# Optimization experiments

Measured on AMD Instinct MI355X. Metric: run time of the kernel, lower is better.

The kernel has to match this reference:

```python
import jax, jax.numpy as jnp
import numpy as np

B = 8; C = 256; NH = 8; CH = C // NH; MLP_H = 4 * C; EPS = 1e-5
SIZES = [(56, 56), (28, 28), (14, 14), (7, 7)]  # scales 2..5; scale1 (112x112) passes through


def _layernorm(x, g, b):
    mu = jnp.mean(x, -1, keepdims=True)
    var = jnp.mean((x - mu) ** 2, -1, keepdims=True)
    return (x - mu) * jax.lax.rsqrt(var + EPS) * g + b


def _dwconv(x, w, b, pad):
    # x: [B, C, H, W], w: [C, 1, k, k] depthwise
    out = jax.lax.conv_general_dilated(
        x, w, (1, 1), [(pad, pad), (pad, pad)],
        feature_group_count=x.shape[1],
        dimension_numbers=('NCHW', 'OIHW', 'NCHW'))
    return out + b[None, :, None, None]


def _cpe(x, w, b, size):
    # ConvPosEnc: depthwise 3x3 conv residual on image tokens, cls untouched
    Hh, Ww = size
    Bb, N, Cc = x.shape
    cls_tok, img = x[:, :1], x[:, 1:]
    feat = img.transpose(0, 2, 1).reshape(Bb, Cc, Hh, Ww)
    feat = _dwconv(feat, w, b, 1) + feat
    img = feat.reshape(Bb, Cc, Hh * Ww).transpose(0, 2, 1)
    return jnp.concatenate([cls_tok, img], axis=1)


def _crpe(q, v, ws, bs, size):
    # ConvRelPosEnc: window->head split {3:2, 5:3, 7:3}; EV_hat = q * dwconv(v)
    Hh, Ww = size
    Bb, h, N, Ch = q.shape
    q_img, v_img = q[:, :, 1:], v[:, :, 1:]
    v_map = v_img.transpose(0, 1, 3, 2).reshape(Bb, h * Ch, Hh, Ww)
    splits = [2 * Ch, 3 * Ch, 3 * Ch]
    start = 0; outs = []
    for i, win in enumerate((3, 5, 7)):
        part = v_map[:, start:start + splits[i]]
        outs.append(_dwconv(part, ws[i], bs[i], win // 2))
        start += splits[i]
    conv_v = jnp.concatenate(outs, 1).reshape(Bb, h, Ch, Hh * Ww).transpose(0, 1, 3, 2)
    ev = q_img * conv_v  # [B, h, HW, Ch]
    return jnp.pad(ev, ((0, 0), (0, 0), (1, 0), (0, 0)))  # zero row for cls token


def _factor_att(x, qkv_w, proj_w, proj_b, crpe_ws, crpe_bs, size):
    Bb, N, Cc = x.shape
    qkv = (x @ qkv_w.T).reshape(Bb, N, 3, NH, CH).transpose(2, 0, 3, 1, 4)
    q, k, v = qkv[0], qkv[1], qkv[2]
    k_sm = jax.nn.softmax(k, axis=2)                       # softmax over tokens
    kv = jnp.einsum('bhnk,bhnv->bhkv', k_sm, v)            # [B,h,Ch,Ch]
    fa = jnp.einsum('bhnk,bhkv->bhnv', q, kv)              # [B,h,N,Ch]
    cr = _crpe(q, v, crpe_ws, crpe_bs, size)
    out = (CH ** -0.5 * fa + cr).transpose(0, 2, 1, 3).reshape(Bb, N, Cc)
    return out @ proj_w.T + proj_b


def _interp(x, out_size, size):
    # bilinear (align_corners=False) on image tokens; cls token passes through
    Bb, N, Cc = x.shape
    Hh, Ww = size
    cls_tok, img = x[:, :1], x[:, 1:]
    feat = img.transpose(0, 2, 1).reshape(Bb, Cc, Hh, Ww)
    feat = jax.image.resize(feat, (Bb, Cc, out_size[0], out_size[1]),
                            method='bilinear', antialias=False)
    img = feat.reshape(Bb, Cc, -1).transpose(0, 2, 1)
    return jnp.concatenate([cls_tok, img], axis=1)


def _mlp(x, w1, b1, w2, b2):
    h = jax.nn.gelu(x @ w1.T + b1, approximate=False)
    return h @ w2.T + b2


def _forward(x1, x2, x3, x4, x5, cpe_w, cpe_b, n1_g, n1_b, qkv_w, proj_w, proj_b,
             crpe_w3, crpe_b3, crpe_w5, crpe_b5, crpe_w7, crpe_b7,
             n2_g, n2_b, fc1_w, fc1_b, fc2_w, fc2_b):
    xs = [x2, x3, x4, x5]
    curs = []
    for i in range(4):  # fixed set of 4 scales (not a data-dim loop)
        xi = _cpe(xs[i], cpe_w[i], cpe_b[i], SIZES[i])
        cur = _layernorm(xi, n1_g[i], n1_b[i])
        cur = _factor_att(cur, qkv_w[i], proj_w[i], proj_b[i],
                          (crpe_w3[i], crpe_w5[i], crpe_w7[i]),
                          (crpe_b3[i], crpe_b5[i], crpe_b7[i]), SIZES[i])
        xs[i] = xi
        curs.append(cur)
    c2, c3, c4, c5 = curs
    s2, s3, s4, s5 = SIZES
    # only the interpolations actually used in the residual sums (source has dead ones)
    c2n = c2 + _interp(c3, s2, s3) + _interp(c4, s2, s4)
    c3n = c3 + _interp(c4, s3, s4) + _interp(c2, s3, s2)
    c4n = c4 + _interp(c5, s4, s5) + _interp(c2, s4, s2)
    c5n = c5 + _interp(c4, s5, s4) + _interp(c2, s5, s2)
    curs = [c2n, c3n, c4n, c5n]
    for i in range(4):
        xs[i] = xs[i] + curs[i]
        cur = _layernorm(xs[i], n2_g[i], n2_b[i])
        cur = _mlp(cur, fc1_w, fc1_b, fc2_w, fc2_b)  # MLP shared across scales
        xs[i] = xs[i] + cur
    return (x1, xs[0], xs[1], xs[2], xs[3])


def setup_inputs() -> dict:
    key = jax.random.key(0)
    ks = iter(jax.random.split(key, 40))
    def nrm(shape, scale=1.0):
        return jax.random.normal(next(ks), shape, jnp.float32) * scale
    W = 0.02
    inp = {}
    inp['x1'] = nrm((B, 1 + 112 * 112, C))
    for j, (h, w) in enumerate(SIZES):
        inp['x%d' % (j + 2)] = nrm((B, 1 + h * w, C))
    inp['cpe_w'] = nrm((4, C, 1, 3, 3), W); inp['cpe_b'] = jnp.zeros((4, C))
    inp['n1_g'] = jnp.ones((4, C)); inp['n1_b'] = jnp.zeros((4, C))
    inp['qkv_w'] = nrm((4, 3 * C, C), W)
    inp['proj_w'] = nrm((4, C, C), W); inp['proj_b'] = jnp.zeros((4, C))
    inp['crpe_w3'] = nrm((4, 2 * CH, 1, 3, 3), W); inp['crpe_b3'] = jnp.zeros((4, 2 * CH))
    inp['crpe_w5'] = nrm((4, 3 * CH, 1, 5, 5), W); inp['crpe_b5'] = jnp.zeros((4, 3 * CH))
    inp['crpe_w7'] = nrm((4, 3 * CH, 1, 7, 7), W); inp['crpe_b7'] = jnp.zeros((4, 3 * CH))
    inp['n2_g'] = jnp.ones((4, C)); inp['n2_b'] = jnp.zeros((4, C))
    inp['fc1_w'] = nrm((MLP_H, C), W); inp['fc1_b'] = jnp.zeros((MLP_H,))
    inp['fc2_w'] = nrm((C, MLP_H), W); inp['fc2_b'] = jnp.zeros((C,))
    return inp


def reference(x1, x2, x3, x4, x5, cpe_w, cpe_b, n1_g, n1_b, qkv_w, proj_w, proj_b,
              crpe_w3, crpe_b3, crpe_w5, crpe_b5, crpe_w7, crpe_b7,
              n2_g, n2_b, fc1_w, fc1_b, fc2_w, fc2_b):
    return _forward(x1, x2, x3, x4, x5, cpe_w, cpe_b, n1_g, n1_b, qkv_w, proj_w, proj_b,
                    crpe_w3, crpe_b3, crpe_w5, crpe_b5, crpe_w7, crpe_b7,
                    n2_g, n2_b, fc1_w, fc1_b, fc2_w, fc2_b)
```

## Files before the change

### kernel.cpp

```cpp
#include <hip/hip_runtime.h>
#include <math.h>

typedef unsigned short u16;
typedef __attribute__((ext_vector_type(8))) short bf16x8;
typedef __attribute__((ext_vector_type(4))) float f32x4;

#define MP 36864
#define OUTOFF0 25692160ull

#define DEV __device__ __forceinline__
#define AS1 __attribute__((address_space(1)))
#define AS3 __attribute__((address_space(3)))

DEV u16 f2bf(float x) {
  union { float f; unsigned u; } v; v.f = x;
  unsigned r = v.u + 0x7fffu + ((v.u >> 16) & 1u);
  return (u16)(r >> 16);
}
DEV float bf2f(u16 x) {
  union { unsigned u; float f; } v; v.u = ((unsigned)x) << 16;
  return v.f;
}

struct alignas(8) u16x4s { u16 x, y, z, w; };
struct alignas(16) U16x8 { u16 d[8]; };

DEV int rs_s(int row)   { return (row >= 25600) + (row >= 33792) + (row >= 35840); }
DEV int selPB(int s)    { return s == 0 ? 0 : s == 1 ? 25600 : s == 2 ? 33792 : 35840; }
DEV int selNPAD(int s)  { return s == 0 ? 3200 : s == 1 ? 1024 : s == 2 ? 256 : 128; }
DEV int selN(int s)     { return s == 0 ? 3137 : s == 1 ? 785 : s == 2 ? 197 : 50; }
DEV int selH(int s)     { return s == 0 ? 56 : s == 1 ? 28 : s == 2 ? 14 : 7; }
DEV int selRO(int s)    { return s == 0 ? 0 : s == 1 ? 25096 : s == 2 ? 31376 : 32952; }
DEV size_t selKPB(int s){ return s == 0 ? 0ull : s == 1 ? 6553600ull : s == 2 ? 8650752ull : 9175040ull; }
DEV size_t selVPB(int s){ return s == 0 ? 0ull : s == 1 ? 7340032ull : s == 2 ? 11010048ull : 12845056ull; }
DEV int selNC(int s)    { return s == 0 ? 32 : s == 1 ? 8 : s == 2 ? 2 : 1; }
DEV int selNCB(int s)   { return s == 0 ? 0 : s == 1 ? 2048 : s == 2 ? 2560 : 2688; }
DEV unsigned selHM(int s){ return s == 0 ? 74899u : s == 1 ? 149797u : s == 2 ? 299594u : 599187u; }

DEV void sbn(int row, int s, int& b, int& n) {
  int l = row - selPB(s);
  if (s == 0)      { b = l / 3200; n = l - b * 3200; }
  else if (s == 1) { b = l >> 10; n = l & 1023; }
  else if (s == 2) { b = l >> 8;  n = l & 255; }
  else             { b = l >> 7;  n = l & 127; }
}

DEV int xcd_swizzle(int orig, int nblk) {
  int q = nblk >> 3, r = nblk & 7;
  int xcd = orig & 7, lin = orig >> 3;
  return (xcd < r ? xcd * (q + 1) : r * (q + 1) + (xcd - r) * q) + lin;
}

__global__ void cvt_bf16(const float* __restrict__ src, u16* __restrict__ dst, int n) {
  for (int i = blockIdx.x * blockDim.x + threadIdx.x; i < n; i += gridDim.x * blockDim.x)
    dst[i] = f2bf(src[i]);
}

__global__ void tpw_cpe(const float* __restrict__ src, float* __restrict__ dst) {
  int i = blockIdx.y;
  int e = blockIdx.x * 256 + threadIdx.x;
  if (e < 2304) {
    int c = e / 9, k = e % 9;
    dst[i * 2304 + k * 256 + c] = src[i * 2304 + c * 9 + k];
  }
}

__global__ void copy_f4(const float4* __restrict__ src, float4* __restrict__ dst, int n4) {
  for (int i = blockIdx.x * blockDim.x + threadIdx.x; i < n4; i += gridDim.x * blockDim.x)
    dst[i] = src[i];
}

__global__ void cpe_ln_all(const float* __restrict__ x2, const float* __restrict__ x3,
                           const float* __restrict__ x4, const float* __restrict__ x5,
                           const float* __restrict__ WT, const float* __restrict__ cpe_b,
                           const float* __restrict__ n1g, const float* __restrict__ n1b,
                           float* __restrict__ XI, u16* __restrict__ T1) {
  int wid = threadIdx.x >> 6, lane = threadIdx.x & 63;
  int row = blockIdx.x * 4 + wid;
  if (row >= MP) return;
  int s = rs_s(row);
  int b, n; sbn(row, s, b, n);
  int N = selN(s), H = selH(s);
  int c4 = lane * 4;
  float4 v = make_float4(0.f, 0.f, 0.f, 0.f);
  if (n < N) {
    const float* x = s == 0 ? x2 : s == 1 ? x3 : s == 2 ? x4 : x5;
    v = *(const float4*)(x + ((size_t)b * N + n) * 256 + c4);
    if (n > 0) {
      int p = n - 1, h0 = p / H, w0 = p % H;
      float4 acc = *(const float4*)(cpe_b + s * 256 + c4);
      const float* wT = WT + s * 2304;
      #pragma unroll
      for (int kh = 0; kh < 3; ++kh) {
        int hh = h0 + kh - 1;
        if (hh < 0 || hh >= H) continue;
        #pragma unroll
        for (int kw = 0; kw < 3; ++kw) {
          int ww = w0 + kw - 1;
          if (ww < 0 || ww >= H) continue;
          float4 t = *(const float4*)(x + ((size_t)b * N + 1 + hh * H + ww) * 256 + c4);
          float4 wv = *(const float4*)(wT + (kh * 3 + kw) * 256 + c4);
          acc.x += t.x * wv.x; acc.y += t.y * wv.y;
          acc.z += t.z * wv.z; acc.w += t.w * wv.w;
        }
      }
      v.x += acc.x; v.y += acc.y; v.z += acc.z; v.w += acc.w;
    }
  }
  *(float4*)(XI + (size_t)row * 256 + c4) = v;
  float sm = v.x + v.y + v.z + v.w;
  #pragma unroll
  for (int off = 32; off; off >>= 1) sm += __shfl_down(sm, off);
  sm = __shfl(sm, 0);
  float mu = sm * (1.0f / 256.0f);
  float dx = v.x - mu, dy = v.y - mu, dz = v.z - mu, dw = v.w - mu;
  float q = dx * dx + dy * dy + dz * dz + dw * dw;
  #pragma unroll
  for (int off = 32; off; off >>= 1) q += __shfl_down(q, off);
  q = __shfl(q, 0);
  float rs = rsqrtf(q * (1.0f / 256.0f) + 1e-5f);
  float4 gg = *(const float4*)(n1g + s * 256 + c4);
  float4 bb = *(const float4*)(n1b + s * 256 + c4);
  u16x4s o;
  o.x = f2bf(dx * rs * gg.x + bb.x);
  o.y = f2bf(dy * rs * gg.y + bb.y);
  o.z = f2bf(dz * rs * gg.z + bb.z);
  o.w = f2bf(dw * rs * gg.w + bb.w);
  *(u16x4s*)(T1 + (size_t)row * 256 + c4) = o;
}

DEV void stage32(const u16* __restrict__ A, const u16* __restrict__ W,
                 u16* dst, int bm, int bn, int K, int k0) {
  int t = threadIdx.x, wv = t >> 6;
  u16* aD = dst;
  u16* bD = dst + 4096;
  #pragma unroll
  for (int iss = 0; iss < 2; ++iss) {
    int sI = iss * 256 + t;
    int row = sI >> 2, g = sI & 3;
    int gel = ((g ^ (row & 3)) << 3);
    __builtin_amdgcn_global_load_lds(
        (const AS1 void*)(A + (size_t)(bm + row) * K + k0 + gel),
        (AS3 void*)(aD + (size_t)(iss * 256 + wv * 64) * 8), 16, 0, 0);
    __builtin_amdgcn_global_load_lds(
        (const AS1 void*)(W + (size_t)(bn + row) * K + k0 + gel),
        (AS3 void*)(bD + (size_t)(iss * 256 + wv * 64) * 8), 16, 0, 0);
  }
}

DEV void mainloop(const u16* __restrict__ A, const u16* __restrict__ W, int K,
                  int bm, int bn, u16* lds, f32x4 (&acc)[4][4]) {
  int t = threadIdx.x, lane = t & 63, wv = t >> 6;
  int wr = wv >> 1, wc = wv & 1;
  const int nt = K >> 5;
  stage32(A, W, lds, bm, bn, K, 0);
  for (int tt = 0; tt < nt; ++tt) {
    __syncthreads();
    if (tt + 1 < nt) stage32(A, W, lds + ((tt + 1) & 1) * 8192, bm, bn, K, (tt + 1) << 5);
    const u16* aS = lds + (tt & 1) * 8192;
    const u16* bS = aS + 4096;
    bf16x8 af[4], bfr[4];
    #pragma unroll
    for (int m = 0; m < 4; ++m) {
      int row = wr * 64 + m * 16 + (lane & 15);
      int sg = (lane >> 4) ^ (row & 3);
      af[m] = *(const bf16x8*)(aS + row * 32 + sg * 8);
    }
    #pragma unroll
    for (int n = 0; n < 4; ++n) {
      int row = wc * 64 + n * 16 + (lane & 15);
      int sg = (lane >> 4) ^ (row & 3);
      bfr[n] = *(const bf16x8*)(bS + row * 32 + sg * 8);
    }
    #pragma unroll
    for (int m = 0; m < 4; ++m)
      #pragma unroll
      for (int n = 0; n < 4; ++n)
        acc[m][n] = __builtin_amdgcn_mfma_f32_16x16x32_bf16(af[m], bfr[n], acc[m][n], 0, 0, 0);
  }
}

DEV void epi_dump(const f32x4 (&acc)[4][4], int pass, float* eps) {
  int t = threadIdx.x, lane = t & 63, wv = t >> 6;
  int wr = wv >> 1, wc = wv & 1;
  if (wr != (pass >> 1)) return;
  #pragma unroll
  for (int mh = 0; mh < 2; ++mh) {
    int m = (pass & 1) * 2 + mh;
    #pragma unroll
    for (int n = 0; n < 4; ++n) {
      int col = wc * 64 + n * 16 + (lane & 15);
      #pragma unroll
      for (int rg = 0; rg < 4; ++rg)
        eps[(mh * 16 + ((lane >> 4) << 2) + rg) * 132 + col] = acc[m][n][rg];
    }
  }
}

template <bool GELU, bool BF16>
DEV void epi_rowmajor(const float* eps, int pass, void* outp, const float* bias,
                      int bm, int bn, int Nout) {
  int t = threadIdx.x;
  int lr = t >> 3, cb = (t & 7) * 4;
  int gr = bm + pass * 32 + lr;
  #pragma unroll
  for (int j = 0; j < 4; ++j) {
    int col = cb + j * 32;
    float4 f = *(const float4*)(eps + lr * 132 + col);
    int gc = bn + col;
    if (bias) {
      float4 bv = *(const float4*)(bias + gc);
      f.x += bv.x; f.y += bv.y; f.z += bv.z; f.w += bv.w;
    }
    if (GELU) {
      f.x /= (1.0f + __expf(-1.702f * f.x));
      f.y /= (1.0f + __expf(-1.702f * f.y));
      f.z /= (1.0f + __expf(-1.702f * f.z));
      f.w /= (1.0f + __expf(-1.702f * f.w));
    }
    if (BF16) {
      u16x4s p;
      p.x = f2bf(f.x); p.y = f2bf(f.y); p.z = f2bf(f.z); p.w = f2bf(f.w);
      *(u16x4s*)((u16*)outp + (size_t)gr * Nout + gc) = p;
    } else {
      *(float4*)((float*)outp + (size_t)gr * Nout + gc) = f;
    }
  }
}

template <bool GELU, bool BF16>
__launch_bounds__(256, 4)
__global__ void gemm_std(const u16* __restrict__ A, const u16* __restrict__ W,
                         const float* __restrict__ bias, void* __restrict__ outp,
                         int K, int Nout, int nnt) {
  __shared__ __align__(16) u16 lds[16384];
  int wg = xcd_swizzle(blockIdx.x, gridDim.x);
  int bm = (wg / nnt) << 7, bn = (wg % nnt) << 7;
  f32x4 acc[4][4] = {};
  mainloop(A, W, K, bm, bn, lds, acc);
  float* eps = (float*)lds;
  #pragma unroll
  for (int pass = 0; pass < 4; ++pass) {
    __syncthreads();
    epi_dump(acc, pass, eps);
    __syncthreads();
    epi_rowmajor<GELU, BF16>(eps, pass, outp, bias, bm, bn, Nout);
  }
}

__launch_bounds__(256, 4)
__global__ void qkv_gemm(const u16* __restrict__ A, const u16* __restrict__ WQ,
                         u16* __restrict__ Q16, u16* __restrict__ KP,
                         u16* __restrict__ VP, u16* __restrict__ VPI) {
  __shared__ __align__(16) u16 lds[16384];
  int wg = xcd_swizzle(blockIdx.x, gridDim.x);
  int mt = wg / 6, ct = wg % 6;
  int bm = mt << 7, bn = ct << 7;
  int s = rs_s(bm);
  f32x4 acc[4][4] = {};
  mainloop(A, WQ + (size_t)s * 196608, 256, bm, bn, lds, acc);
  float* eps = (float*)lds;
  int b, nb; sbn(bm, s, b, nb);
  int NPAD = selNPAD(s), H = selH(s), HW = H * H;
  unsigned hmag = selHM(s);
  #pragma unroll
  for (int pass = 0; pass < 4; ++pass) {
    __syncthreads();
    epi_dump(acc, pass, eps);
    __syncthreads();
    if (ct < 2) {
      epi_rowmajor<false, true>(eps, pass, Q16, nullptr, bm, bn, 256);
    } else {
      int t = threadIdx.x;
      int c = t >> 1, half = t & 1;
      bool isK = (ct < 4);
      int cg = bn - (isK ? 256 : 512) + c;
      int n0 = nb + pass * 32 + half * 16;
      float vals[16];
      #pragma unroll
      for (int r = 0; r < 16; ++r) vals[r] = eps[(half * 16 + r) * 132 + c];
      U16x8 p0, p1;
      #pragma unroll
      for (int e = 0; e < 8; ++e) { p0.d[e] = f2bf(vals[e]); p1.d[e] = f2bf(vals[8 + e]); }
      u16* pbase = (isK ? KP : VP) + selKPB(s) + (size_t)(b * 256 + cg) * NPAD + n0;
      *(U16x8*)pbase = p0;
      *(U16x8*)(pbase + 8) = p1;
      if (!isK) {
        u16* vplane = VPI + selVPB(s) + (size_t)(b * 256 + cg) * (H * 64);
        #pragma unroll
        for (int r = 0; r < 16; ++r) {
          int n = n0 + r;
          if (n >= 1 && n <= HW) {
            int p = n - 1;
            int qd = (int)(((unsigned)p * hmag) >> 22);
            vplane[qd * 64 + (p - qd * H)] = f2bf(vals[r]);
          }
        }
      }
    }
  }
}

__launch_bounds__(256, 4)
__global__ void proj_gemm(const u16* __restrict__ A, const u16* __restrict__ WP,
                          const float* __restrict__ proj_b, float* __restrict__ CC) {
  __shared__ __align__(16) u16 lds[16384];
  int wg = xcd_swizzle(blockIdx.x, gridDim.x);
  int bm = (wg >> 1) << 7, bn = (wg & 1) << 7;
  int s = rs_s(bm);
  f32x4 acc[4][4] = {};
  mainloop(A, WP + (size_t)s * 65536, 256, bm, bn, lds, acc);
  float* eps = (float*)lds;
  #pragma unroll
  for (int pass = 0; pass < 4; ++pass) {
    __syncthreads();
    epi_dump(acc, pass, eps);
    __syncthreads();
    epi_rowmajor<false, false>(eps, pass, CC, proj_b + s * 256, bm, bn, 256);
  }
}

__launch_bounds__(256, 4)
__global__ void fc2_gemm(const u16* __restrict__ A, const u16* __restrict__ W2,
                         const float* __restrict__ fc2_b, const float* __restrict__ XI,
                         float* __restrict__ out) {
  __shared__ __align__(16) u16 lds[16384];
  int wg = xcd_swizzle(blockIdx.x, gridDim.x);
  int bm = (wg >> 1) << 7, bn = (wg & 1) << 7;
  f32x4 acc[4][4] = {};
  mainloop(A, W2, 1024, bm, bn, lds, acc);
  float* eps = (float*)lds;
  int s = rs_s(bm);
  int b, nb; sbn(bm, s, b, nb);
  int N = selN(s), RO = selRO(s);
  #pragma unroll
  for (int pass = 0; pass < 4; ++pass) {
    __syncthreads();
    epi_dump(acc, pass, eps);
    __syncthreads();
    int t = threadIdx.x;
    int lr = t >> 3, cb = (t & 7) * 4;
    int n = nb + pass * 32 + lr;
    if (n >= N) continue;
    int prow = bm + pass * 32 + lr;
    size_t orow = (size_t)RO + (size_t)b * N + n;
    #pragma unroll
    for (int j = 0; j < 4; ++j) {
      int col = cb + j * 32;
      float4 f = *(const float4*)(eps + lr * 132 + col);
      int gc = bn + col;
      float4 bv = *(const float4*)(fc2_b + gc);
      float4 rv = *(const float4*)(XI + (size_t)prow * 256 + gc);
      f.x += bv.x + rv.x; f.y += bv.y + rv.y;
      f.z += bv.z + rv.z; f.w += bv.w + rv.w;
      *(float4*)(out + OUTOFF0 + orow * 256 + gc) = f;
    }
  }
}

__global__ void ksm_all(const u16* __restrict__ KP, float* __restrict__ mx,
                        float* __restrict__ se) {
  int s = blockIdx.z, b = blockIdx.y;
  int N = selN(s), NPAD = selNPAD(s);
  int wv = threadIdx.x >> 6, lane = threadIdx.x & 63;
  int cg = blockIdx.x * 4 + wv;
  const u16* kp = KP + selKPB(s) + (size_t)(b * 256 + cg) * NPAD;
  float m = -1e30f, sm = 0.f;
  for (int n = lane; n < N; n += 64) {
    float v = bf2f(kp[n]);
    float nm = fmaxf(m, v);
    sm = sm * __expf(m - nm) + __expf(v - nm);
    m = nm;
  }
  #pragma unroll
  for (int off = 1; off < 64; off <<= 1) {
    float mo = __shfl_xor(m, off), so = __shfl_xor(sm, off);
    float nm = fmaxf(m, mo);
    sm = sm * __expf(m - nm) + so * __expf(mo - nm);
    m = nm;
  }
  if (lane == 0) { mx[s * 2048 + b * 256 + cg] = m; se[s * 2048 + b * 256 + cg] = sm; }
}

__launch_bounds__(1024)
__global__ void kv_partial_all(const u16* __restrict__ KP, const u16* __restrict__ VP,
                               const float* __restrict__ mx, float* __restrict__ part) {
  __shared__ float kl[32][65];
  __shared__ float vl[32][65];
  int blk = blockIdx.x;
  int s = (blk >= selNCB(1)) + (blk >= selNCB(2)) + (blk >= selNCB(3));
  int local = blk - selNCB(s);
  int NC = selNC(s);
  int chunk = local % NC;
  int bh = local / NC;
  int b = bh >> 3, h = bh & 7;
  int N = selN(s), NPAD = selNPAD(s);
  int chunkrows = (N + NC - 1) / NC;
  const u16* kpb = KP + selKPB(s);
  const u16* vpb = VP + selKPB(s);
  int t = threadIdx.x;
  int i = t >> 5, j = t & 31;
  float acc = 0.f;
  int n0s = chunk * chunkrows, n1s = min(N, n0s + chunkrows);
  for (int n0 = n0s; n0 < n1s; n0 += 64) {
    #pragma unroll
    for (int e = t; e < 2048; e += 1024) {
      int c = e >> 6, nn = e & 63;
      int n = n0 + nn;
      bool ok = (n < n1s);
      kl[c][nn] = ok ? bf2f(kpb[(size_t)(b * 256 + h * 32 + c) * NPAD + n]) : -1e30f;
      vl[c][nn] = ok ? bf2f(vpb[(size_t)(b * 256 + h * 32 + c) * NPAD + n]) : 0.f;
    }
    __syncthreads();
    #pragma unroll
    for (int e = t; e < 2048; e += 1024) {
      int c = e >> 6, nn = e & 63;
      kl[c][nn] = __expf(kl[c][nn] - mx[s * 2048 + b * 256 + h * 32 + c]);
    }
    __syncthreads();
    #pragma unroll
    for (int nn = 0; nn < 64; ++nn) acc += kl[i][nn] * vl[j][nn];
    __syncthreads();
  }
  part[(size_t)blk * 1024 + t] = acc;
}

__global__ void kv_reduce_all(const float* __restrict__ part, const float* __restrict__ se,
                              float* __restrict__ kv) {
  int bh = blockIdx.x, s = blockIdx.y;
  int NC = selNC(s), base = selNCB(s);
  int t = threadIdx.x;
  int i = t >> 5;
  int b = bh >> 3, h = bh & 7;
  float sm = 0.f;
  for (int c = 0; c < NC; ++c) sm += part[(size_t)(base + bh * NC + c) * 1024 + t];
  kv[(size_t)s * 65536 + bh * 1024 + t] = sm / se[s * 2048 + b * 256 + h * 32 + i];
}

template <int KS, int C0>
__global__ void crpe_all(const u16* __restrict__ VPI, const float* __restrict__ w,
                         const float* __restrict__ bias, u16* __restrict__ CVPI, int CS) {
  constexpr int pad = KS / 2;
  int z = blockIdx.z;
  int s = (z >= 2) + (z >= 3) + (z >= 4);
  int sub = z - (s == 0 ? 0 : s + 1);
  int RS = (s == 0) ? 2 : 1;
  int H = selH(s);
  int c = blockIdx.x, b = blockIdx.y;
  int G = (H + 7) >> 3;
  int hpb = (H + RS - 1) / RS;
  int h0b = sub * hpb;
  int h1b = min(H, h0b + hpb);
  size_t plane = selVPB(s) + (size_t)(b * 256 + C0 + c) * (size_t)(H * 64);
  const u16* vp = VPI + plane;
  u16* op = CVPI + plane;
  float wreg[KS * KS];
  #pragma unroll
  for (int e = 0; e < KS * KS; ++e) wreg[e] = w[(s * CS + c) * KS * KS + e];
  float bb = bias[s * CS + c];
  int ntask = (h1b - h0b) * G;
  for (int task = threadIdx.x; task < ntask; task += 256) {
    int g = task % G;
    int h = h0b + task / G;
    int w0 = g << 3;
    float o[8];
    #pragma unroll
    for (int e = 0; e < 8; ++e) o[e] = bb;
    #pragma unroll
    for (int kh = 0; kh < KS; ++kh) {
      int hh = h + kh - pad;
      if (hh < 0 || hh >= H) continue;
      const u16* rowp = vp + hh * 64;
      U16x8 ch0 = {}, ch1, ch2;
      if (w0 >= 8) ch0 = *(const U16x8*)(rowp + w0 - 8);
      ch1 = *(const U16x8*)(rowp + w0);
      ch2 = *(const U16x8*)(rowp + w0 + 8);
      float tv[24];
      #pragma unroll
      for (int j2 = 8 - pad; j2 <= 15 + pad; ++j2) {
        u16 raw = (j2 < 8) ? ch0.d[j2] : (j2 < 16 ? ch1.d[j2 - 8] : ch2.d[j2 - 16]);
        tv[j2] = bf2f(raw);
      }
      #pragma unroll
      for (int kw = 0; kw < KS; ++kw) {
        float wv = wreg[kh * KS + kw];
        #pragma unroll
        for (int e = 0; e < 8; ++e) o[e] += tv[8 + e + kw - pad] * wv;
      }
    }
    U16x8 pk;
    #pragma unroll
    for (int e = 0; e < 8; ++e) pk.d[e] = f2bf(o[e]);
    *(U16x8*)(op + h * 64 + w0) = pk;
  }
}

__global__ void att_all(const u16* __restrict__ Q16, const u16* __restrict__ CVPI,
                        const float* __restrict__ kvg, u16* __restrict__ attp) {
  int s = blockIdx.z, b = blockIdx.y;
  int N = selN(s), H = selH(s);
  int n0 = blockIdx.x * 16;
  if (n0 >= N) return;
  __shared__ float kvl[8192];
  __shared__ float ql[256];
  __shared__ float cl[16][260];
  int t = threadIdx.x;
  int hw64 = H * 64;
  size_t rowbase = (size_t)selPB(s) + (size_t)b * selNPAD(s);
  const u16* cvb = CVPI + selVPB(s);
  for (int e = t; e < 8192; e += 256) kvl[e] = kvg[(size_t)s * 65536 + b * 8192 + e];
  for (int e = t; e < 4096; e += 256) {
    int c = e >> 4, nn = e & 15;
    int n = n0 + nn;
    float v = 0.f;
    if (n >= 1 && n < N) {
      int p = n - 1;
      v = bf2f(cvb[(size_t)(b * 256 + c) * hw64 + (p / H) * 64 + (p % H)]);
    }
    cl[nn][c] = v;
  }
  int h = t >> 5, j = t & 31;
  for (int nn = 0; nn < 16; ++nn) {
    int n = n0 + nn;
    if (n >= N) break;
    __syncthreads();
    ql[t] = bf2f(Q16[(rowbase + n) * 256 + t]);
    __syncthreads();
    float fa = 0.f;
    const float* kvh = kvl + h * 1024;
    #pragma unroll
    for (int k = 0; k < 32; ++k) fa += ql[h * 32 + k] * kvh[k * 32 + j];
    float v = 0.17677669529663687f * fa + ql[t] * cl[nn][t];
    attp[(rowbase + n) * 256 + t] = f2bf(v);
  }
}

DEV float4 bs4(const float* __restrict__ base, int Hs, int oh, int ow, int Hi, int c4) {
  float scale = (float)Hs / (float)Hi;
  float sy = (oh + 0.5f) * scale - 0.5f;
  float sx = (ow + 0.5f) * scale - 0.5f;
  float fy0 = floorf(sy), fx0 = floorf(sx);
  float fy = sy - fy0, fx = sx - fx0;
  int y0 = (int)fy0, x0 = (int)fx0;
  int y0c = min(max(y0, 0), Hs - 1), y1c = min(max(y0 + 1, 0), Hs - 1);
  int x0c = min(max(x0, 0), Hs - 1), x1c = min(max(x0 + 1, 0), Hs - 1);
  const float* ib = base + 256 + c4;
  float4 v00 = *(const float4*)(ib + (size_t)(y0c * Hs + x0c) * 256);
  float4 v01 = *(const float4*)(ib + (size_t)(y0c * Hs + x1c) * 256);
  float4 v10 = *(const float4*)(ib + (size_t)(y1c * Hs + x0c) * 256);
  float4 v11 = *(const float4*)(ib + (size_t)(y1c * Hs + x1c) * 256);
  float w00 = (1.f - fy) * (1.f - fx), w01 = (1.f - fy) * fx;
  float w10 = fy * (1.f - fx), w11 = fy * fx;
  float4 r;
  r.x = w00 * v00.x + w01 * v01.x + w10 * v10.x + w11 * v11.x;
  r.y = w00 * v00.y + w01 * v01.y + w10 * v10.y + w11 * v11.y;
  r.z = w00 * v00.z + w01 * v01.z + w10 * v10.z + w11 * v11.z;
  r.w = w00 * v00.w + w01 * v01.w + w10 * v10.w + w11 * v11.w;
  return r;
}

__global__ void combine_ln_all(float* __restrict__ XI, const float* __restrict__ CC,
                               const float* __restrict__ n2g, const float* __restrict__ n2b,
                               u16* __restrict__ T1) {
  int wid = threadIdx.x >> 6, lane = threadIdx.x & 63;
  int row = blockIdx.x * 4 + wid;
  if (row >= MP) return;
  int s = rs_s(row);
  int b, n; sbn(row, s, b, n);
  int N = selN(s), Hi = selH(s);
  int c4 = lane * 4;
  float4 v;
  if (n < N) {
    float4 add = *(const float4*)(CC + (size_t)row * 256 + c4);
    int sa = s == 0 ? 1 : s == 1 ? 2 : s == 2 ? 3 : 2;
    int sb_ = s == 0 ? 2 : 0;
    const float* baseA = CC + ((size_t)selPB(sa) + (size_t)b * selNPAD(sa)) * 256;
    const float* baseB = CC + ((size_t)selPB(sb_) + (size_t)b * selNPAD(sb_)) * 256;
    if (n == 0) {
      float4 a = *(const float4*)(baseA + c4);
      float4 bb2 = *(const float4*)(baseB + c4);
      add.x += a.x + bb2.x; add.y += a.y + bb2.y;
      add.z += a.z + bb2.z; add.w += a.w + bb2.w;
    } else {
      int p = n - 1, oh = p / Hi, ow = p % Hi;
      float4 a = bs4(baseA, selH(sa), oh, ow, Hi, c4);
      float4 bb2 = bs4(baseB, selH(sb_), oh, ow, Hi, c4);
      add.x += a.x + bb2.x; add.y += a.y + bb2.y;
      add.z += a.z + bb2.z; add.w += a.w + bb2.w;
    }
    float* xp = XI + (size_t)row * 256 + c4;
    v = *(const float4*)xp;
    v.x += add.x; v.y += add.y; v.z += add.z; v.w += add.w;
    *(float4*)xp = v;
  } else {
    v = make_float4(0.f, 0.f, 0.f, 0.f);
  }
  float sm = v.x + v.y + v.z + v.w;
  #pragma unroll
  for (int off = 32; off; off >>= 1) sm += __shfl_down(sm, off);
  sm = __shfl(sm, 0);
  float mu = sm * (1.0f / 256.0f);
  float dx = v.x - mu, dy = v.y - mu, dz = v.z - mu, dw = v.w - mu;
  float q = dx * dx + dy * dy + dz * dz + dw * dw;
  #pragma unroll
  for (int off = 32; off; off >>= 1) q += __shfl_down(q, off);
  q = __shfl(q, 0);
  float rs = rsqrtf(q * (1.0f / 256.0f) + 1e-5f);
  float4 gg = *(const float4*)(n2g + s * 256 + c4);
  float4 bb = *(const float4*)(n2b + s * 256 + c4);
  u16x4s o;
  o.x = f2bf(dx * rs * gg.x + bb.x);
  o.y = f2bf(dy * rs * gg.y + bb.y);
  o.z = f2bf(dz * rs * gg.z + bb.z);
  o.w = f2bf(dw * rs * gg.w + bb.w);
  *(u16x4s*)(T1 + (size_t)row * 256 + c4) = o;
}

extern "C" void kernel_launch(void* const* d_in, const int* in_sizes, int n_in,
                              void* d_out, int out_size, void* d_ws, size_t ws_size,
                              hipStream_t stream) {
  const float* x1 = (const float*)d_in[0];
  const float* x2 = (const float*)d_in[1];
  const float* x3 = (const float*)d_in[2];
  const float* x4 = (const float*)d_in[3];
  const float* x5 = (const float*)d_in[4];
  const float* cpe_w  = (const float*)d_in[5];
  const float* cpe_b  = (const float*)d_in[6];
  const float* n1_g   = (const float*)d_in[7];
  const float* n1_b   = (const float*)d_in[8];
  const float* qkv_w  = (const float*)d_in[9];
  const float* proj_w = (const float*)d_in[10];
  const float* proj_b = (const float*)d_in[11];
  const float* crpe_w3 = (const float*)d_in[12];
  const float* crpe_b3 = (const float*)d_in[13];
  const float* crpe_w5 = (const float*)d_in[14];
  const float* crpe_b5 = (const float*)d_in[15];
  const float* crpe_w7 = (const float*)d_in[16];
  const float* crpe_b7 = (const float*)d_in[17];
  const float* n2_g   = (const float*)d_in[18];
  const float* n2_b   = (const float*)d_in[19];
  const float* fc1_w  = (const float*)d_in[20];
  const float* fc1_b  = (const float*)d_in[21];
  const float* fc2_w  = (const float*)d_in[22];
  const float* fc2_b  = (const float*)d_in[23];

  float* ws = (float*)d_ws;
  float* XI   = ws;
  float* CC   = XI + 9437184;
  u16*   T1   = (u16*)(CC + 9437184);
  float* REG  = (float*)(T1 + 9437184);
  u16*   Q16  = (u16*)REG;
  u16*   KP   = Q16 + 9437184;
  u16*   VP   = KP + 9437184;
  u16*   VPI  = VP + 9437184;
  u16*   CVPI = VPI + 13762560;
  float* PRT  = (float*)CVPI;
  u16*   T2   = (u16*)REG;
  float* MX   = (float*)(CVPI + 13762560);
  float* SE   = MX + 8192;
  float* KV   = SE + 8192;
  u16*   WQ   = (u16*)(KV + 262144);
  u16*   WP   = WQ + 786432;
  u16*   W1   = WP + 262144;
  u16*   W2   = W1 + 262144;
  float* WT   = (float*)(W2 + 262144);

  float* out = (float*)d_out;

  hipMemsetAsync(VPI, 0, 13762560ull * 2, stream);
  cvt_bf16<<<1536, 256, 0, stream>>>(qkv_w, WQ, 786432);
  cvt_bf16<<<512, 256, 0, stream>>>(proj_w, WP, 262144);
  cvt_bf16<<<512, 256, 0, stream>>>(fc1_w, W1, 262144);
  cvt_bf16<<<512, 256, 0, stream>>>(fc2_w, W2, 262144);
  tpw_cpe<<<dim3(9, 4), 256, 0, stream>>>(cpe_w, WT);

  copy_f4<<<8192, 256, 0, stream>>>((const float4*)x1, (float4*)out, 25692160 / 4);

  cpe_ln_all<<<MP / 4, 256, 0, stream>>>(x2, x3, x4, x5, WT, cpe_b, n1_g, n1_b, XI, T1);

  qkv_gemm<<<288 * 6, 256, 0, stream>>>(T1, WQ, Q16, KP, VP, VPI);

  ksm_all<<<dim3(64, 8, 4), 256, 0, stream>>>(KP, MX, SE);
  kv_partial_all<<<2752, 1024, 0, stream>>>(KP, VP, MX, PRT);
  kv_reduce_all<<<dim3(64, 4), 1024, 0, stream>>>(PRT, SE, KV);
  crpe_all<3, 0><<<dim3(64, 8, 5), 256, 0, stream>>>(VPI, crpe_w3, crpe_b3, CVPI, 64);
  crpe_all<5, 64><<<dim3(96, 8, 5), 256, 0, stream>>>(VPI, crpe_w5, crpe_b5, CVPI, 96);
  crpe_all<7, 160><<<dim3(96, 8, 5), 256, 0, stream>>>(VPI, crpe_w7, crpe_b7, CVPI, 96);
  att_all<<<dim3(197, 8, 4), 256, 0, stream>>>(Q16, CVPI, KV, T1);

  proj_gemm<<<288 * 2, 256, 0, stream>>>(T1, WP, proj_b, CC);

  combine_ln_all<<<MP / 4, 256, 0, stream>>>(XI, CC, n2_g, n2_b, T1);

  gemm_std<true, true><<<288 * 8, 256, 0, stream>>>(T1, W1, fc1_b, (void*)T2, 256, 1024, 8);
  fc2_gemm<<<288 * 2, 256, 0, stream>>>(T2, W2, fc2_b, XI, out);
}
```

Before: 489.3 us.

## Triple-buffer GEMM mainloop, fuse weight casts, move V image scatter to own kernel

The shared GEMM mainloop moves from double to triple buffering. It waits on explicit vmcnt counters and a raw barrier so two K-tiles of loads stay in flight, which uses more LDS and lowers launch bounds to 3 blocks per SM. The four weight conversion launches are merged into one kernel. The memset of the padded V image is replaced by a separate vimg_fill kernel that reads VP and writes the padded planes with zero fill, taking the scattered 16-bit stores out of the QKV epilogue at the cost of an extra read pass.

```diff
diff --git a/kernel.cpp b/kernel.cpp
--- a/kernel.cpp
+++ b/kernel.cpp
@@ -35,7 +35,6 @@
 DEV size_t selVPB(int s){ return s == 0 ? 0ull : s == 1 ? 7340032ull : s == 2 ? 11010048ull : 12845056ull; }
 DEV int selNC(int s)    { return s == 0 ? 32 : s == 1 ? 8 : s == 2 ? 2 : 1; }
 DEV int selNCB(int s)   { return s == 0 ? 0 : s == 1 ? 2048 : s == 2 ? 2560 : 2688; }
-DEV unsigned selHM(int s){ return s == 0 ? 74899u : s == 1 ? 149797u : s == 2 ? 299594u : 599187u; }
 
 DEV void sbn(int row, int s, int& b, int& n) {
   int l = row - selPB(s);
@@ -51,9 +50,15 @@
   return (xcd < r ? xcd * (q + 1) : r * (q + 1) + (xcd - r) * q) + lin;
 }
 
-__global__ void cvt_bf16(const float* __restrict__ src, u16* __restrict__ dst, int n) {
-  for (int i = blockIdx.x * blockDim.x + threadIdx.x; i < n; i += gridDim.x * blockDim.x)
-    dst[i] = f2bf(src[i]);
+__global__ void cvt_all(const float* __restrict__ qkv_w, const float* __restrict__ proj_w,
+                        const float* __restrict__ fc1_w, const float* __restrict__ fc2_w,
+                        u16* __restrict__ WQ, u16* __restrict__ WP,
+                        u16* __restrict__ W1, u16* __restrict__ W2) {
+  int i = blockIdx.x * 256 + threadIdx.x;
+  if (i < 786432) WQ[i] = f2bf(qkv_w[i]);
+  else if (i < 1048576) WP[i - 786432] = f2bf(proj_w[i - 786432]);
+  else if (i < 1310720) W1[i - 1048576] = f2bf(fc1_w[i - 1048576]);
+  else if (i < 1572864) W2[i - 1310720] = f2bf(fc2_w[i - 1310720]);
 }
 
 __global__ void tpw_cpe(const float* __restrict__ src, float* __restrict__ dst) {
@@ -154,10 +159,18 @@
   int wr = wv >> 1, wc = wv & 1;
   const int nt = K >> 5;
   stage32(A, W, lds, bm, bn, K, 0);
+  stage32(A, W, lds + 8192, bm, bn, K, 32);
+  int buf = 0;
   for (int tt = 0; tt < nt; ++tt) {
-    __syncthreads();
-    if (tt + 1 < nt) stage32(A, W, lds + ((tt + 1) & 1) * 8192, bm, bn, K, (tt + 1) << 5);
-    const u16* aS = lds + (tt & 1) * 8192;
+    if (tt + 1 < nt) asm volatile("s_waitcnt vmcnt(4)" ::: "memory");
+    else             asm volatile("s_waitcnt vmcnt(0)" ::: "memory");
+    __builtin_amdgcn_s_barrier();
+    asm volatile("" ::: "memory");
+    if (tt + 2 < nt) {
+      int nb = buf + 2; if (nb >= 3) nb -= 3;
+      stage32(A, W, lds + nb * 8192, bm, bn, K, (tt + 2) << 5);
+    }
+    const u16* aS = lds + buf * 8192;
     const u16* bS = aS + 4096;
     bf16x8 af[4], bfr[4];
     #pragma unroll
@@ -177,6 +190,7 @@
       #pragma unroll
       for (int n = 0; n < 4; ++n)
         acc[m][n] = __builtin_amdgcn_mfma_f32_16x16x32_bf16(af[m], bfr[n], acc[m][n], 0, 0, 0);
+    buf += 1; if (buf >= 3) buf -= 3;
   }
 }
 
@@ -229,11 +243,11 @@
 }
 
 template <bool GELU, bool BF16>
-__launch_bounds__(256, 4)
+__launch_bounds__(256, 3)
 __global__ void gemm_std(const u16* __restrict__ A, const u16* __restrict__ W,
                          const float* __restrict__ bias, void* __restrict__ outp,
                          int K, int Nout, int nnt) {
-  __shared__ __align__(16) u16 lds[16384];
+  __shared__ __align__(16) u16 lds[24576];
   int wg = xcd_swizzle(blockIdx.x, gridDim.x);
   int bm = (wg / nnt) << 7, bn = (wg % nnt) << 7;
   f32x4 acc[4][4] = {};
@@ -248,11 +262,11 @@
   }
 }
 
-__launch_bounds__(256, 4)
+__launch_bounds__(256, 3)
 __global__ void qkv_gemm(const u16* __restrict__ A, const u16* __restrict__ WQ,
                          u16* __restrict__ Q16, u16* __restrict__ KP,
-                         u16* __restrict__ VP, u16* __restrict__ VPI) {
-  __shared__ __align__(16) u16 lds[16384];
+                         u16* __restrict__ VP) {
+  __shared__ __align__(16) u16 lds[24576];
   int wg = xcd_swizzle(blockIdx.x, gridDim.x);
   int mt = wg / 6, ct = wg % 6;
   int bm = mt << 7, bn = ct << 7;
@@ -261,8 +275,7 @@
   mainloop(A, WQ + (size_t)s * 196608, 256, bm, bn, lds, acc);
   float* eps = (float*)lds;
   int b, nb; sbn(bm, s, b, nb);
-  int NPAD = selNPAD(s), H = selH(s), HW = H * H;
-  unsigned hmag = selHM(s);
+  int NPAD = selNPAD(s);
   #pragma unroll
   for (int pass = 0; pass < 4; ++pass) {
     __syncthreads();
@@ -285,26 +298,14 @@
       u16* pbase = (isK ? KP : VP) + selKPB(s) + (size_t)(b * 256 + cg) * NPAD + n0;
       *(U16x8*)pbase = p0;
       *(U16x8*)(pbase + 8) = p1;
-      if (!isK) {
-        u16* vplane = VPI + selVPB(s) + (size_t)(b * 256 + cg) * (H * 64);
-        #pragma unroll
-        for (int r = 0; r < 16; ++r) {
-          int n = n0 + r;
-          if (n >= 1 && n <= HW) {
-            int p = n - 1;
-            int qd = (int)(((unsigned)p * hmag) >> 22);
-            vplane[qd * 64 + (p - qd * H)] = f2bf(vals[r]);
-          }
-        }
-      }
-    }
-  }
-}
-
-__launch_bounds__(256, 4)
+    }
+  }
+}
+
+__launch_bounds__(256, 3)
 __global__ void proj_gemm(const u16* __restrict__ A, const u16* __restrict__ WP,
                           const float* __restrict__ proj_b, float* __restrict__ CC) {
-  __shared__ __align__(16) u16 lds[16384];
+  __shared__ __align__(16) u16 lds[24576];
   int wg = xcd_swizzle(blockIdx.x, gridDim.x);
   int bm = (wg >> 1) << 7, bn = (wg & 1) << 7;
   int s = rs_s(bm);
@@ -320,11 +321,11 @@
   }
 }
 
-__launch_bounds__(256, 4)
+__launch_bounds__(256, 3)
 __global__ void fc2_gemm(const u16* __restrict__ A, const u16* __restrict__ W2,
                          const float* __restrict__ fc2_b, const float* __restrict__ XI,
                          float* __restrict__ out) {
-  __shared__ __align__(16) u16 lds[16384];
+  __shared__ __align__(16) u16 lds[24576];
   int wg = xcd_swizzle(blockIdx.x, gridDim.x);
   int bm = (wg >> 1) << 7, bn = (wg & 1) << 7;
   f32x4 acc[4][4] = {};
@@ -355,6 +356,20 @@
       f.z += bv.z + rv.z; f.w += bv.w + rv.w;
       *(float4*)(out + OUTOFF0 + orow * 256 + gc) = f;
     }
+  }
+}
+
+__global__ void vimg_fill(const u16* __restrict__ VP, u16* __restrict__ VPI) {
+  int plane = blockIdx.x;
+  int s = plane >> 11;
+  int pc = plane & 2047;
+  int H = selH(s), NPAD = selNPAD(s);
+  const u16* vp = VP + selKPB(s) + (size_t)pc * NPAD;
+  u16* vi = VPI + selVPB(s) + (size_t)pc * (H * 64);
+  int tot = H * 64;
+  for (int e = threadIdx.x; e < tot; e += 256) {
+    int h = e >> 6, w = e & 63;
+    vi[e] = (w < H) ? vp[1 + h * H + w] : (u16)0;
   }
 }
 
@@ -667,18 +682,15 @@
 
   float* out = (float*)d_out;
 
-  hipMemsetAsync(VPI, 0, 13762560ull * 2, stream);
-  cvt_bf16<<<1536, 256, 0, stream>>>(qkv_w, WQ, 786432);
-  cvt_bf16<<<512, 256, 0, stream>>>(proj_w, WP, 262144);
-  cvt_bf16<<<512, 256, 0, stream>>>(fc1_w, W1, 262144);
-  cvt_bf16<<<512, 256, 0, stream>>>(fc2_w, W2, 262144);
+  cvt_all<<<6144, 256, 0, stream>>>(qkv_w, proj_w, fc1_w, fc2_w, WQ, WP, W1, W2);
   tpw_cpe<<<dim3(9, 4), 256, 0, stream>>>(cpe_w, WT);
 
   copy_f4<<<8192, 256, 0, stream>>>((const float4*)x1, (float4*)out, 25692160 / 4);
 
   cpe_ln_all<<<MP / 4, 256, 0, stream>>>(x2, x3, x4, x5, WT, cpe_b, n1_g, n1_b, XI, T1);
 
-  qkv_gemm<<<288 * 6, 256, 0, stream>>>(T1, WQ, Q16, KP, VP, VPI);
+  qkv_gemm<<<288 * 6, 256, 0, stream>>>(T1, WQ, Q16, KP, VP);
+  vimg_fill<<<8192, 256, 0, stream>>>(VP, VPI);
 
   ksm_all<<<dim3(64, 8, 4), 256, 0, stream>>>(KP, MX, SE);
   kv_partial_all<<<2752, 1024, 0, stream>>>(KP, VP, MX, PRT);
```

Measured after the change: 446.5 us. 8.8% less time.
